# Optimization experiments

Hardware: AMD Instinct MI355X
Metric: run time of the kernel (lower is better)

## Reference

```python
import jax, jax.numpy as jnp
import numpy as np

B, SEQ, PRED, N, PATCH, STRIDE = 4, 720, 720, 64, 16, 8
DM, EL = 256, 2
PNUM = (PRED + SEQ - PATCH) // STRIDE + 2  # 180
EPS = 1e-5


def _gelu(x):
    return jax.nn.gelu(x, approximate=False)  # torch nn.GELU default (erf)


def _ln(x, w, b):
    mu = x.mean(-1, keepdims=True)
    var = ((x - mu) ** 2).mean(-1, keepdims=True)
    return (x - mu) / jnp.sqrt(var + EPS) * w + b


def _pos_emb(n, d):
    pos = np.arange(n)[:, None].astype(np.float32)
    div = np.exp(np.arange(0, d, 2).astype(np.float32) * (-np.log(10000.0) / d))
    pe = np.zeros((n, d), np.float32)
    pe[:, 0::2] = np.sin(pos * div)
    pe[:, 1::2] = np.cos(pos * div)
    return jnp.asarray(pe)


def _patch_embed(x, emb_w):
    # x: [B, N, L]; ReplicationPad1d((0, STRIDE)) then unfold(patch_len, stride)
    xp = jnp.concatenate([x, jnp.repeat(x[..., -1:], STRIDE, axis=-1)], axis=-1)
    npatch = (xp.shape[-1] - PATCH) // STRIDE + 1
    idx = jnp.arange(npatch)[:, None] * STRIDE + jnp.arange(PATCH)[None, :]
    patches = xp[..., idx]  # [B, N, npatch, PATCH]
    emb = jnp.einsum('bnpl,ld->bnpd', patches, emb_w) + _pos_emb(npatch, DM)
    return emb.reshape(-1, npatch, DM)  # [B*N, npatch, DM]


def _temp_mix(x, w1, b1, w2, b2, nw, nb):
    # Pnum independent Linear(DM,DM)->GELU->Linear(DM,DM), residual + LayerNorm
    h = _gelu(jnp.einsum('bpd,pde->bpe', x, w1) + b1[None])
    o = jnp.einsum('bpd,pde->bpe', h, w2) + b2[None]
    return _ln(o + x, nw, nb)


def _chan_mix(x, w1, b1, w2, b2, nw, nb):
    # DM independent Linear(PNUM,PNUM)->GELU->Linear(PNUM,PNUM), residual + LayerNorm
    h = _gelu(jnp.einsum('bpd,dpq->bqd', x, w1) + b1.T[None])
    o = jnp.einsum('bpd,dpq->bqd', h, w2) + b2.T[None]
    return _ln(o + x, nw, nb)


def _s_correction(x, x_pre):
    xf = jnp.fft.rfft(x, axis=1, norm='ortho')
    pf = jnp.fft.rfft(x_pre, axis=1, norm='ortho')
    xi = jnp.maximum(jnp.fft.irfft(xf * jnp.conj(xf), axis=1), 0.0)
    pi = jnp.maximum(jnp.fft.irfft(pf * jnp.conj(pf), axis=1), 0.0)
    alpha = (xi * pi).sum(1, keepdims=True) / ((pi * pi).sum(1, keepdims=True) + 0.001)
    return jnp.sqrt(alpha)


def _forward(history_data, future_data, revin_w, revin_b, pred_w, pred_b, emb_w,
             ln_w, ln_b, comb_w, comb_b, head_w, head_b,
             tmd_w1, tmd_b1, tmd_w2, tmd_b2, tmd_nw, tmd_nb,
             cmd_w1, cmd_b1, cmd_w2, cmd_b2, cmd_nw, cmd_nb,
             tmu_w1, tmu_b1, tmu_w2, tmu_b2, tmu_nw, tmu_nb,
             cmu_w1, cmu_b1, cmu_w2, cmu_b2, cmu_nw, cmu_nb):
    x0 = history_data[:, :, :, 0]  # [B, SEQ, N]
    mean = x0.mean(1, keepdims=True)
    stdev = jnp.sqrt(x0.var(1, keepdims=True) + EPS)  # unbiased=False
    xn = (x0 - mean) / stdev * revin_w + revin_b  # RevIN norm (affine)
    x = jnp.einsum('bln,lt->bnt', xn, pred_w) + pred_b  # predict_linear on [B,N,SEQ]
    xi = _patch_embed(x, emb_w)  # [B*N, PNUM, DM]
    x_old = _patch_embed(jnp.transpose(x0, (0, 2, 1)), emb_w)  # [B*N, P_old, DM]
    x_all = jnp.zeros(xi.shape + (EL,), xi.dtype)
    for li in range(EL):
        xud = _temp_mix(xi, tmd_w1[li], tmd_b1[li], tmd_w2[li], tmd_b2[li], tmd_nw[li], tmd_nb[li])
        xud = _chan_mix(xud, cmd_w1[li], cmd_b1[li], cmd_w2[li], cmd_b2[li], cmd_nw[li], cmd_nb[li])
        for j in range(li, -1, -1):
            xud = _temp_mix(xud, tmu_w1[j], tmu_b1[j], tmu_w2[j], tmu_b2[j], tmu_nw[j], tmu_nb[j])
            xud = _chan_mix(xud, cmu_w1[j], cmu_b1[j], cmu_w2[j], cmu_b2[j], cmu_nw[j], cmu_nb[j])
        # faithful to original: inner loop shadows `i`, so the write index is always 0
        x_all = x_all.at[:, :, :, 0].set(xud)
    xc = jnp.einsum('bpde,e->bpd', x_all, comb_w) + comb_b  # comb: Linear(EL, 1)
    p_old = x_old.shape[1]
    xc = _s_correction(_ln(x_old, ln_w, ln_b), _ln(xc[:, :p_old, :], ln_w, ln_b)) * xc
    xr = xc.reshape(-1, N, PNUM, DM).transpose(0, 1, 3, 2)  # [B, N, DM, PNUM]
    out = xr.reshape(xr.shape[0], N, DM * PNUM) @ head_w + head_b  # Flatten_Head -> [B, N, PRED]
    out = jnp.transpose(out, (0, 2, 1))  # [B, PRED, N]
    out = (out - revin_b) / (revin_w + EPS * EPS) * stdev + mean  # RevIN denorm
    return out[:, -PRED:, :][..., None]  # [B, PRED, N, 1]


def setup_inputs() -> dict:
    key = jax.random.key(0)
    ks = iter(jax.random.split(key, 64))
    f = lambda shape, s=0.02: s * jax.random.normal(next(ks), shape, jnp.float32)
    inp = dict(
        history_data=jax.random.normal(next(ks), (B, SEQ, N, 1), jnp.float32),
        future_data=jax.random.normal(next(ks), (B, PRED, N, 1), jnp.float32),
        batch_seen=0, epoch=0, train=0,
        revin_w=jnp.ones((N,), jnp.float32), revin_b=jnp.zeros((N,), jnp.float32),
        pred_w=f((SEQ, SEQ + PRED)), pred_b=jnp.zeros((SEQ + PRED,), jnp.float32),
        emb_w=f((PATCH, DM)),
        ln_w=jnp.ones((DM,), jnp.float32), ln_b=jnp.zeros((DM,), jnp.float32),
        comb_w=f((EL,), 0.5), comb_b=jnp.zeros((), jnp.float32),
        head_w=f((DM * PNUM, PRED), 0.005), head_b=jnp.zeros((PRED,), jnp.float32),
    )
    for pre in ('tmd', 'tmu'):
        inp[pre + '_w1'] = f((EL, PNUM, DM, DM)); inp[pre + '_b1'] = jnp.zeros((EL, PNUM, DM), jnp.float32)
        inp[pre + '_w2'] = f((EL, PNUM, DM, DM)); inp[pre + '_b2'] = jnp.zeros((EL, PNUM, DM), jnp.float32)
        inp[pre + '_nw'] = jnp.ones((EL, DM), jnp.float32); inp[pre + '_nb'] = jnp.zeros((EL, DM), jnp.float32)
    for pre in ('cmd', 'cmu'):
        inp[pre + '_w1'] = f((EL, DM, PNUM, PNUM)); inp[pre + '_b1'] = jnp.zeros((EL, DM, PNUM), jnp.float32)
        inp[pre + '_w2'] = f((EL, DM, PNUM, PNUM)); inp[pre + '_b2'] = jnp.zeros((EL, DM, PNUM), jnp.float32)
        inp[pre + '_nw'] = jnp.ones((EL, DM), jnp.float32); inp[pre + '_nb'] = jnp.zeros((EL, DM), jnp.float32)
    return inp


def reference(history_data, future_data, revin_w, revin_b, pred_w, pred_b, emb_w,
              ln_w, ln_b, comb_w, comb_b, head_w, head_b,
              tmd_w1, tmd_b1, tmd_w2, tmd_b2, tmd_nw, tmd_nb,
              cmd_w1, cmd_b1, cmd_w2, cmd_b2, cmd_nw, cmd_nb,
              tmu_w1, tmu_b1, tmu_w2, tmu_b2, tmu_nw, tmu_nb,
              cmu_w1, cmu_b1, cmu_w2, cmu_b2, cmu_nw, cmu_nb,
              batch_seen, epoch, train):
    return _forward(history_data, future_data, revin_w, revin_b, pred_w, pred_b, emb_w,
                    ln_w, ln_b, comb_w, comb_b, head_w, head_b,
                    tmd_w1, tmd_b1, tmd_w2, tmd_b2, tmd_nw, tmd_nb,
                    cmd_w1, cmd_b1, cmd_w2, cmd_b2, cmd_nw, cmd_nb,
                    tmu_w1, tmu_b1, tmu_w2, tmu_b2, tmu_nw, tmu_nb,
                    cmu_w1, cmu_b1, cmu_w2, cmu_b2, cmu_nw, cmu_nb)
```

## Files before the change

### kernel.cpp

```cpp
#include <hip/hip_runtime.h>
#include <cstdint>
#include <cstddef>

namespace {

constexpr int SEQ_ = 720;
constexpr int N_ = 64;
constexpr int T_ = 1440;
constexpr int P_ = 180;
constexpr int PO_ = 90;
constexpr int D_ = 256;
constexpr int PD_ = P_ * D_;
constexpr float EPS_ = 1e-5f;
constexpr int NTILE_ = 39744;

typedef __attribute__((ext_vector_type(8))) short bf16x8;
typedef __attribute__((ext_vector_type(4))) float f32x4;
typedef __attribute__((ext_vector_type(4))) unsigned short u16x4;

__device__ __forceinline__ float gelu_exact(float x) {
  return 0.5f * x * (1.0f + erff(x * 0.70710678118654752f));
}

__device__ __forceinline__ unsigned short f2bf(float x) {
// ... 115 lines not shown
      int idx = bn * 90 + p0 + tid;
      muX[idx] = mu;
      rsX[idx] = rsqrtf(Q * (1.f / 256.f) - mu * mu + EPS_);
    }
  }
}

struct TileInfo {
  const float* Wg; unsigned short* Og;
  int K, Nn, Kp, k0, n0;
};

__device__ __forceinline__ TileInfo decode_tile(
    int bid,
    const float* t0, const float* t1, const float* t2, const float* t3,
    const float* t4, const float* t5,
    const float* c0, const float* c1, const float* c2, const float* c3,
    const float* c4p, const float* c5, const float* hw,
    unsigned short* WtAll, unsigned short* WcAll, unsigned short* WhAll) {
  TileInfo ti;
  int tk, tn;
  if (bid < 17280) {
    int tt = bid / 2880, rem = bid - tt * 2880;
    int g = rem >> 4, tile = rem & 15;
    const float* s = t0;
    if (tt == 1) s = t1; else if (tt == 2) s = t2; else if (tt == 3) s = t3;
    else if (tt == 4) s = t4; else if (tt == 5) s = t5;
    ti.Wg = s + (size_t)g * 65536;
    ti.Og = WtAll + (size_t)tt * 11796480 + (size_t)g * 65536;
    ti.K = 256; ti.Nn = 256; ti.Kp = 256; tk = tile >> 2; tn = tile & 3;
  } else if (bid < 31104) {
    int b2 = bid - 17280;
    int tt = b2 / 2304, rem = b2 - tt * 2304;
    int g = rem / 9, tile = rem - g * 9;
    const float* s = c0;
    if (tt == 1) s = c1; else if (tt == 2) s = c2; else if (tt == 3) s = c3;
    else if (tt == 4) s = c4p; else if (tt == 5) s = c5;
    ti.Wg = s + (size_t)g * 32400;
    ti.Og = WcAll + (size_t)tt * 9437184 + (size_t)g * 36864;
    ti.K = 180; ti.Nn = 180; ti.Kp = 192; tk = tile / 3; tn = tile - (tile / 3) * 3;
  } else {
    int b2 = bid - 31104;
    ti.Wg = hw; ti.Og = WhAll;
    ti.K = 46080; ti.Nn = 720; ti.Kp = 46080; tk = b2 / 12; tn = b2 - (b2 / 12) * 12;
  }
  ti.k0 = tk * 64; ti.n0 = tn * 64;
  return ti;
}

__global__ __launch_bounds__(256) void convT_all_kernel(
    const float* t0, const float* t1, const float* t2, const float* t3,
    const float* t4, const float* t5,
    const float* c0, const float* c1, const float* c2, const float* c3,
    const float* c4p, const float* c5,
    const float* hw,
    unsigned short* WtAll, unsigned short* WcAll, unsigned short* WhAll,
    int phase, int step) {
  __shared__ float Ts[2][64][65];
  int tid = threadIdx.x;
  int kr = tid >> 4, nc = (tid & 15) * 4;
  int S = gridDim.x * step;

  auto do_load = [&](const TileInfo& ti, float4* r) {
    #pragma unroll
    for (int i = 0; i < 4; i++) {
      int k = ti.k0 + kr + i * 16;
      float4 v = make_float4(0.f, 0.f, 0.f, 0.f);
      if (k < ti.K) {
        int n = ti.n0 + nc;
        if (n + 3 < ti.Nn) {
          v = *reinterpret_cast<const float4*>(ti.Wg + (size_t)k * ti.Nn + n);
        } else {
          if (n + 0 < ti.Nn) v.x = ti.Wg[(size_t)k * ti.Nn + n + 0];
          if (n + 1 < ti.Nn) v.y = ti.Wg[(size_t)k * ti.Nn + n + 1];
          if (n + 2 < ti.Nn) v.z = ti.Wg[(size_t)k * ti.Nn + n + 2];
          if (n + 3 < ti.Nn) v.w = ti.Wg[(size_t)k * ti.Nn + n + 3];
        }
      }
      r[i] = v;
    }
  };

  auto do_write = [&](const float4* r, int b) {
    #pragma unroll
    for (int i = 0; i < 4; i++) {
      Ts[b][kr + i * 16][nc + 0] = r[i].x;
      Ts[b][kr + i * 16][nc + 1] = r[i].y;
      Ts[b][kr + i * 16][nc + 2] = r[i].z;
      Ts[b][kr + i * 16][nc + 3] = r[i].w;
    }
  };

  auto do_store = [&](const TileInfo& ti, int b) {
    #pragma unroll
    for (int it = 0; it < 2; it++) {
      int nr = (tid >> 3) + it * 32;
      int kc = (tid & 7) * 8;
      unsigned int tmp[4];
      #pragma unroll
      for (int j = 0; j < 4; j++) {
        unsigned int lo = f2bf(Ts[b][kc + 2 * j][nr]);
        unsigned int hi = f2bf(Ts[b][kc + 2 * j + 1][nr]);
        tmp[j] = lo | (hi << 16);
      }
      uint4 vv; vv.x = tmp[0]; vv.y = tmp[1]; vv.z = tmp[2]; vv.w = tmp[3];
      *reinterpret_cast<uint4*>(ti.Og + (size_t)(ti.n0 + nr) * ti.Kp + ti.k0 + kc) = vv;
    }
  };

#define DECODE(tt) decode_tile((tt), t0,t1,t2,t3,t4,t5, c0,c1,c2,c3,c4p,c5, hw, WtAll, WcAll, WhAll)

  int t = phase + blockIdx.x * step;
  if (t >= NTILE_) return;

  float4 rA[4], rB[4];
  TileInfo i0 = DECODE(t);
  do_load(i0, rA);
  bool v1 = (t + S < NTILE_);
  TileInfo i1 = v1 ? DECODE(t + S) : i0;
  if (v1) do_load(i1, rB);
  do_write(rA, 0);
  bool v2 = (t + 2 * S < NTILE_);
  TileInfo i2 = v2 ? DECODE(t + 2 * S) : i0;
  if (v2) do_load(i2, rA);
  __syncthreads();

  while (true) {
    if (v1) do_write(rB, 1);
    {
      bool v3 = (t + 3 * S < NTILE_);
      TileInfo i3 = i2;
      if (v3) { i3 = DECODE(t + 3 * S); do_load(i3, rB); }
      do_store(i0, 0);
      __syncthreads();
      t += S;
      if (!v1) return;
      i0 = i1; i1 = i2; i2 = i3; v1 = v2; v2 = v3;
    }
    if (v1) do_write(rA, 0);
    {
      bool v3 = (t + 3 * S < NTILE_);
      TileInfo i3 = i2;
      if (v3) { i3 = DECODE(t + 3 * S); do_load(i3, rA); }
      do_store(i0, 1);
      __syncthreads();
      t += S;
      if (!v1) return;
      i0 = i1; i1 = i2; i2 = i3; v1 = v2; v2 = v3;
    }
  }
#undef DECODE
}

__global__ __launch_bounds__(256, 3) void temp_mfma_kernel(
    const unsigned short* __restrict__ X, unsigned short* __restrict__ Y,
    const unsigned short* __restrict__ W1t, const float* __restrict__ B1,
    const unsigned short* __restrict__ W2t, const float* __restrict__ B2,
    const float* __restrict__ NW, const float* __restrict__ NB) {
  __shared__ __align__(16) short Xs[64 * 256];
  __shared__ float partS[64][4];
  __shared__ float partQ[64][4];
  int lin = (blockIdx.x & 7) * 90 + (blockIdx.x >> 3);
  int p = lin >> 2;
  int m0 = (lin & 3) << 6;
  int tid = threadIdx.x;
  int w = tid >> 6, l = tid & 63;
  int lr = l & 15, lq = l >> 4;
  int n0w = w << 6;

  const unsigned short* W1p = W1t + (size_t)p * 65536;
  const unsigned short* W2p = W2t + (size_t)p * 65536;

  bf16x8 bhc[4], bhn[4];
  #pragma unroll
  for (int nf = 0; nf < 4; nf++)
    bhc[nf] = *reinterpret_cast<const bf16x8*>(W1p + (size_t)(n0w + nf * 16 + lr) * 256 + lq * 8);

  const unsigned short* Xblk = X + (size_t)m0 * PD_ + (size_t)p * D_;
  for (int i = tid; i < 64 * 32; i += 256) {
    int r = i >> 5, c8 = (i & 31) << 3;
    uint4 v = *reinterpret_cast<const uint4*>(Xblk + (size_t)r * PD_ + c8);
    *reinterpret_cast<uint4*>(&Xs[r * 256 + (c8 ^ ((r & 7) << 3))]) = v;
  }
  __syncthreads();

  f32x4 zero4 = {0.f, 0.f, 0.f, 0.f};
  f32x4 acc[4][4];
  #pragma unroll
  for (int a = 0; a < 4; a++)
    #pragma unroll
    for (int b = 0; b < 4; b++) acc[a][b] = zero4;

  for (int ks = 0; ks < 8; ks++) {
    int kb = ks * 32 + lq * 8;
    bf16x8 af[4];
    #pragma unroll
    for (int mf = 0; mf < 4; mf++) {
      int r = mf * 16 + lr;
      af[mf] = *reinterpret_cast<const bf16x8*>(&Xs[r * 256 + (kb ^ ((r & 7) << 3))]);
    }
    if (ks < 7) {
      #pragma unroll
      for (int nf = 0; nf < 4; nf++)
        bhn[nf] = *reinterpret_cast<const bf16x8*>(W1p + (size_t)(n0w + nf * 16 + lr) * 256 + kb + 32);
    }
    #pragma unroll
    for (int mf = 0; mf < 4; mf++)
      #pragma unroll
      for (int nf = 0; nf < 4; nf++)
        acc[mf][nf] = __builtin_amdgcn_mfma_f32_16x16x32_bf16(af[mf], bhc[nf], acc[mf][nf], 0, 0, 0);
    if (ks < 7) {
      #pragma unroll
      for (int nf = 0; nf < 4; nf++) bhc[nf] = bhn[nf];
    }
  }

  bf16x8 bh2[4];
  #pragma unroll
  for (int nf = 0; nf < 4; nf++)
    bh2[nf] = *reinterpret_cast<const bf16x8*>(W2p + (size_t)(n0w + nf * 16 + lr) * 256 + lq * 8);

  __syncthreads();

  #pragma unroll
  for (int nf = 0; nf < 4; nf++) {
    int n = n0w + nf * 16 + lr;
    float bias = B1[p * 256 + n];
    #pragma unroll
    for (int mf = 0; mf < 4; mf++)
      #pragma unroll
      for (int rg = 0; rg < 4; rg++) {
        int r = mf * 16 + lq * 4 + rg;
        Xs[r * 256 + (n ^ ((r & 7) << 3))] =
            (short)f2bf(gelu_exact(acc[mf][nf][rg] + bias));
      }
  }
  __syncthreads();

  #pragma unroll
  for (int a = 0; a < 4; a++)
    #pragma unroll
    for (int b = 0; b < 4; b++) acc[a][b] = zero4;
  for (int ks = 0; ks < 8; ks++) {
    int kb = ks * 32 + lq * 8;
    bf16x8 af[4];
    #pragma unroll
    for (int mf = 0; mf < 4; mf++) {
      int r = mf * 16 + lr;
      af[mf] = *reinterpret_cast<const bf16x8*>(&Xs[r * 256 + (kb ^ ((r & 7) << 3))]);
    }
    if (ks < 7) {
      #pragma unroll
      for (int nf = 0; nf < 4; nf++)
        bhn[nf] = *reinterpret_cast<const bf16x8*>(W2p + (size_t)(n0w + nf * 16 + lr) * 256 + kb + 32);
    }
    #pragma unroll
    for (int mf = 0; mf < 4; mf++)
      #pragma unroll
      for (int nf = 0; nf < 4; nf++)
        acc[mf][nf] = __builtin_amdgcn_mfma_f32_16x16x32_bf16(af[mf], bh2[nf], acc[mf][nf], 0, 0, 0);
    if (ks < 7) {
      #pragma unroll
      for (int nf = 0; nf < 4; nf++) bh2[nf] = bhn[nf];
    }
  }

  __syncthreads();

  for (int i = tid; i < 64 * 32; i += 256) {
    int r = i >> 5, c8 = (i & 31) << 3;
    uint4 v = *reinterpret_cast<const uint4*>(Xblk + (size_t)r * PD_ + c8);
    *reinterpret_cast<uint4*>(&Xs[r * 256 + (c8 ^ ((r & 7) << 3))]) = v;
  }
  __syncthreads();

  float b2v[4], nwv[4], nbv[4];
  #pragma unroll
  for (int nf = 0; nf < 4; nf++) {
    int n = n0w + nf * 16 + lr;
    b2v[nf] = B2[p * 256 + n];
    nwv[nf] = NW[n];
    nbv[nf] = NB[n];
  }
  #pragma unroll
  for (int nf = 0; nf < 4; nf++) {
    int n = n0w + nf * 16 + lr;
    #pragma unroll
    for (int mf = 0; mf < 4; mf++)
      #pragma unroll
      for (int rg = 0; rg < 4; rg++) {
        int r = mf * 16 + lq * 4 + rg;
        float res = bf2f((unsigned short)Xs[r * 256 + (n ^ ((r & 7) << 3))]);
        acc[mf][nf][rg] += b2v[nf] + res;
      }
  }
  #pragma unroll
  for (int mf = 0; mf < 4; mf++)
    #pragma unroll
    for (int rg = 0; rg < 4; rg++) {
      float s = acc[mf][0][rg] + acc[mf][1][rg] + acc[mf][2][rg] + acc[mf][3][rg];
      float q = acc[mf][0][rg] * acc[mf][0][rg] + acc[mf][1][rg] * acc[mf][1][rg] +
                acc[mf][2][rg] * acc[mf][2][rg] + acc[mf][3][rg] * acc[mf][3][rg];
      #pragma unroll
      for (int off = 1; off < 16; off <<= 1) {
        s += __shfl_xor(s, off);
        q += __shfl_xor(q, off);
      }
      if (lr == 0) {
        int r = mf * 16 + lq * 4 + rg;
        partS[r][w] = s;
        partQ[r][w] = q;
      }
    }
  __syncthreads();
  #pragma unroll
  for (int mf = 0; mf < 4; mf++)
    #pragma unroll
    for (int rg = 0; rg < 4; rg++) {
      int r = mf * 16 + lq * 4 + rg;
      float S = partS[r][0] + partS[r][1] + partS[r][2] + partS[r][3];
      float Q = partQ[r][0] + partQ[r][1] + partQ[r][2] + partQ[r][3];
      float mu = S * (1.f / 256.f);
      float rstd = rsqrtf(Q * (1.f / 256.f) - mu * mu + EPS_);
      #pragma unroll
      for (int nf = 0; nf < 4; nf++) {
        int n = n0w + nf * 16 + lr;
        Xs[r * 256 + (n ^ ((r & 7) << 3))] =
            (short)f2bf((acc[mf][nf][rg] - mu) * rstd * nwv[nf] + nbv[nf]);
      }
    }
  __syncthreads();
  unsigned short* Yblk = Y + (size_t)m0 * PD_ + (size_t)p * D_;
  for (int i = tid; i < 64 * 32; i += 256) {
    int r = i >> 5, c8 = (i & 31) << 3;
    uint4 v = *reinterpret_cast<uint4*>(&Xs[r * 256 + (c8 ^ ((r & 7) << 3))]);
    *reinterpret_cast<uint4*>(Yblk + (size_t)r * PD_ + c8) = v;
  }
}

__global__ __launch_bounds__(256) void tr_AB_kernel(
    const unsigned short* __restrict__ A, unsigned short* __restrict__ B16) {
  __shared__ unsigned short T[32][184];
  int bn = blockIdx.y;
  int d0 = blockIdx.x * 32;
  int tid = threadIdx.x;
  int ld = tid & 31, pw = tid >> 5;
  for (int p = pw; p < 180; p += 8)
    T[ld][p] = A[((size_t)bn * 180 + p) * 256 + d0 + ld];
  __syncthreads();
  unsigned int* Bu = reinterpret_cast<unsigned int*>(B16);
  for (int i = tid; i < 32 * 96; i += 256) {
    int r = i / 96, jj = i - r * 96;
    int p0 = 2 * jj;
    unsigned int lo = (p0 < 180) ? (unsigned int)T[r][p0] : 0u;
    unsigned int hi = (p0 + 1 < 180) ? (unsigned int)T[r][p0 + 1] : 0u;
    Bu[((size_t)bn * 256 + d0 + r) * 96 + jj] = lo | (hi << 16);
  }
}

__global__ __launch_bounds__(256, 3) void chan_mfma_kernel(
    const unsigned short* __restrict__ Xb, unsigned short* __restrict__ Yb,
    const unsigned short* __restrict__ W1t, const float* __restrict__ B1,
    const unsigned short* __restrict__ W2t, const float* __restrict__ B2) {
  __shared__ __align__(16) short Xs[64 * 200];
  int lin = (blockIdx.x & 7) * 128 + (blockIdx.x >> 3);
  int d = lin >> 2;
  int m0 = (lin & 3) << 6;
  int tid = threadIdx.x;
  int w = tid >> 6, l = tid & 63;
  int lr = l & 15, lq = l >> 4;
  int n0w = w * 48;

  const unsigned short* W1p = W1t + (size_t)d * (192 * 192);
  const unsigned short* W2p = W2t + (size_t)d * (192 * 192);

  bf16x8 bhc[3], bhn[3];
  #pragma unroll
  for (int nf = 0; nf < 3; nf++)
    bhc[nf] = *reinterpret_cast<const bf16x8*>(W1p + (size_t)(n0w + nf * 16 + lr) * 192 + lq * 8);

  for (int i = tid; i < 64 * 24; i += 256) {
    int r = i / 24, c = i - r * 24;
    uint4 v = *reinterpret_cast<const uint4*>(
        Xb + ((size_t)(m0 + r) * 256 + d) * 192 + c * 8);
    *reinterpret_cast<uint4*>(&Xs[r * 200 + c * 8]) = v;
  }
  __syncthreads();

  f32x4 zero4 = {0.f, 0.f, 0.f, 0.f};
  f32x4 acc[4][3];
  #pragma unroll
  for (int a = 0; a < 4; a++)
    #pragma unroll
    for (int b = 0; b < 3; b++) acc[a][b] = zero4;

  for (int ks = 0; ks < 6; ks++) {
    int kb = ks * 32 + lq * 8;
    bf16x8 af[4];
    #pragma unroll
    for (int mf = 0; mf < 4; mf++)
      af[mf] = *reinterpret_cast<const bf16x8*>(&Xs[(mf * 16 + lr) * 200 + kb]);
    if (ks < 5) {
      #pragma unroll
      for (int nf = 0; nf < 3; nf++)
        bhn[nf] = *reinterpret_cast<const bf16x8*>(W1p + (size_t)(n0w + nf * 16 + lr) * 192 + kb + 32);
    }
    #pragma unroll
    for (int mf = 0; mf < 4; mf++)
      #pragma unroll
      for (int nf = 0; nf < 3; nf++)
        acc[mf][nf] = __builtin_amdgcn_mfma_f32_16x16x32_bf16(af[mf], bhc[nf], acc[mf][nf], 0, 0, 0);
    if (ks < 5) {
      #pragma unroll
      for (int nf = 0; nf < 3; nf++) bhc[nf] = bhn[nf];
    }
  }

  bf16x8 bh2[3];
  #pragma unroll
  for (int nf = 0; nf < 3; nf++)
    bh2[nf] = *reinterpret_cast<const bf16x8*>(W2p + (size_t)(n0w + nf * 16 + lr) * 192 + lq * 8);

  __syncthreads();

  #pragma unroll
  for (int nf = 0; nf < 3; nf++) {
    int n = n0w + nf * 16 + lr;
    bool valid = n < 180;
    float bias = valid ? B1[d * 180 + n] : 0.f;
    #pragma unroll
    for (int mf = 0; mf < 4; mf++)
      #pragma unroll
      for (int rg = 0; rg < 4; rg++) {
        int r = mf * 16 + lq * 4 + rg;
        float h = valid ? gelu_exact(acc[mf][nf][rg] + bias) : 0.f;
        Xs[r * 200 + n] = (short)f2bf(h);
      }
  }
  __syncthreads();

  #pragma unroll
  for (int a = 0; a < 4; a++)
    #pragma unroll
    for (int b = 0; b < 3; b++) acc[a][b] = zero4;
  for (int ks = 0; ks < 6; ks++) {
    int kb = ks * 32 + lq * 8;
    bf16x8 af[4];
    #pragma unroll
    for (int mf = 0; mf < 4; mf++)
      af[mf] = *reinterpret_cast<const bf16x8*>(&Xs[(mf * 16 + lr) * 200 + kb]);
    if (ks < 5) {
      #pragma unroll
      for (int nf = 0; nf < 3; nf++)
        bhn[nf] = *reinterpret_cast<const bf16x8*>(W2p + (size_t)(n0w + nf * 16 + lr) * 192 + kb + 32);
    }
    #pragma unroll
    for (int mf = 0; mf < 4; mf++)
      #pragma unroll
      for (int nf = 0; nf < 3; nf++)
        acc[mf][nf] = __builtin_amdgcn_mfma_f32_16x16x32_bf16(af[mf], bh2[nf], acc[mf][nf], 0, 0, 0);
    if (ks < 5) {
      #pragma unroll
      for (int nf = 0; nf < 3; nf++) bh2[nf] = bhn[nf];
    }
  }

  __syncthreads();

  for (int i = tid; i < 64 * 24; i += 256) {
    int r = i / 24, c = i - r * 24;
    uint4 v = *reinterpret_cast<const uint4*>(
        Xb + ((size_t)(m0 + r) * 256 + d) * 192 + c * 8);
    *reinterpret_cast<uint4*>(&Xs[r * 200 + c * 8]) = v;
  }
  __syncthreads();

  #pragma unroll
  for (int nf = 0; nf < 3; nf++) {
    int n = n0w + nf * 16 + lr;
    if (n < 180) {
      float b2v = B2[d * 180 + n];
      #pragma unroll
      for (int mf = 0; mf < 4; mf++)
        #pragma unroll
        for (int rg = 0; rg < 4; rg++) {
          int r = mf * 16 + lq * 4 + rg;
          float res = bf2f((unsigned short)Xs[r * 200 + n]);
          Yb[((size_t)(m0 + r) * 256 + d) * 180 + n] = f2bf(acc[mf][nf][rg] + b2v + res);
        }
    }
  }
}

__global__ __launch_bounds__(256) void trLN_kernel(
    const unsigned short* __restrict__ Bsrc, unsigned short* __restrict__ A,
    const float* __restrict__ nw, const float* __restrict__ nb,
    const float* __restrict__ cw, const float* __restrict__ cb, int useComb,
    float* __restrict__ muP, float* __restrict__ rsP) {
  __shared__ float Tl[16][260];
  int bn = blockIdx.y;
  int p0 = blockIdx.x * 16;
  int tid = threadIdx.x;
  int j = tid & 15, db = tid >> 4;
  #pragma unroll 4
  for (int it = 0; it < 16; ++it) {
    int dd = it * 16 + db;
    float v = 0.f;
    if (p0 + j < 180)
      v = bf2f(Bsrc[((size_t)(bn * 256) + dd) * 180 + p0 + j]);
    Tl[j][dd] = v;
  }
  __syncthreads();
  int w = tid >> 6, l = tid & 63;
  float scale = 1.f, shift = 0.f;
  if (useComb) { scale = cw[0]; shift = cb[0]; }
  float4 w4 = *reinterpret_cast<const float4*>(nw + l * 4);
  float4 b4 = *reinterpret_cast<const float4*>(nb + l * 4);
  #pragma unroll
  for (int rr = 0; rr < 4; ++rr) {
    int row = w * 4 + rr;
    int p = p0 + row;
    float4 v = *reinterpret_cast<const float4*>(&Tl[row][l * 4]);
    float s = v.x + v.y + v.z + v.w;
    float s2 = v.x*v.x + v.y*v.y + v.z*v.z + v.w*v.w;
    #pragma unroll
    for (int off = 32; off > 0; off >>= 1) { s += __shfl_xor(s, off); s2 += __shfl_xor(s2, off); }
    float mu = s * (1.f/256.f);
    float rstd = rsqrtf(s2 * (1.f/256.f) - mu * mu + EPS_);
    if (p < 180) {
      float o0 = ((v.x - mu) * rstd * w4.x + b4.x) * scale + shift;
      float o1 = ((v.y - mu) * rstd * w4.y + b4.y) * scale + shift;
      float o2 = ((v.z - mu) * rstd * w4.z + b4.z) * scale + shift;
      float o3 = ((v.w - mu) * rstd * w4.w + b4.w) * scale + shift;
      unsigned int w0 = (unsigned int)f2bf(o0) | ((unsigned int)f2bf(o1) << 16);
      unsigned int w1 = (unsigned int)f2bf(o2) | ((unsigned int)f2bf(o3) << 16);
      unsigned int* dst = reinterpret_cast<unsigned int*>(
          A + ((size_t)bn * 180 + p) * 256 + l * 4);
      dst[0] = w0; dst[1] = w1;
      if (useComb && p < 90) {
        float so = o0 + o1 + o2 + o3;
        float qo = o0*o0 + o1*o1 + o2*o2 + o3*o3;
        #pragma unroll
        for (int off = 32; off > 0; off >>= 1) { so += __shfl_xor(so, off); qo += __shfl_xor(qo, off); }
        if (l == 0) {
          float muo = so * (1.f/256.f);
          muP[bn * 90 + p] = muo;
          rsP[bn * 90 + p] = rsqrtf(qo * (1.f/256.f) - muo * muo + EPS_);
        }
      }
    }
  }
}

__global__ __launch_bounds__(128, 1) void autocorr_kernel(
    const unsigned short* __restrict__ xoldB, const unsigned short* __restrict__ xcB,
    const float* __restrict__ muX, const float* __restrict__ rsX,
    const float* __restrict__ muP, const float* __restrict__ rsP,
    const float* __restrict__ lnw, const float* __restrict__ lnb,
    float* __restrict__ sqa) {
  __shared__ float PI[46][64];
  __shared__ float RED[2][2][64];
  int bn = blockIdx.x >> 2;
  int tid = threadIdx.x;
  int dl = tid & 63;
  int half = tid >> 6;
  int j0 = half * 23;
  int d = ((blockIdx.x & 3) << 6) + dl;
  float w = lnw[d], bb = lnb[d];
  float v[90], wr[90];

  {
    const unsigned short* col = xcB + (size_t)bn * PD_ + d;
    const float* m = muP + bn * 90;
    const float* rs = rsP + bn * 90;
    #pragma unroll
    for (int p = 0; p < 90; p++)
      v[p] = (bf2f(col[(size_t)p * D_]) - m[p]) * rs[p] * w + bb;
    #pragma unroll
    for (int p = 0; p < 90; p++)
      wr[p] = (half == 0) ? v[p] : v[(p + 23) % 90];
  }
  float den = 0.f;
  #pragma unroll 1
  for (int jt = 0; jt < 24; jt += 4) {
    float c0 = 0.f, c1 = 0.f, c2 = 0.f, c3 = 0.f;
    #pragma unroll
    for (int mm = 0; mm < 90; mm++) {
      float vm = v[mm];
      c0 += vm * wr[mm];
      c1 += vm * ((mm + 1 < 90) ? wr[mm + 1] : wr[mm - 89]);
      c2 += vm * ((mm + 2 < 90) ? wr[mm + 2] : wr[mm - 88]);
      c3 += vm * ((mm + 3 < 90) ? wr[mm + 3] : wr[mm - 87]);
    }
    float cq[4] = {c0, c1, c2, c3};
    #pragma unroll
    for (int q = 0; q < 4; q++) {
      if (jt + q < 23) {
        int lag = j0 + jt + q;
        float piv = fmaxf(cq[q] * 0.10540925533894598f, 0.f);
        PI[lag][dl] = piv;
        float wgt = (lag == 0 || lag == 45) ? 1.f : 2.f;
        den += wgt * piv * piv;
      }
    }
    float t0 = wr[0], t1 = wr[1], t2 = wr[2], t3 = wr[3];
    #pragma unroll
    for (int mm = 0; mm < 86; mm++) wr[mm] = wr[mm + 4];
    wr[86] = t0; wr[87] = t1; wr[88] = t2; wr[89] = t3;
  }

  {
    const unsigned short* col = xoldB + (size_t)bn * (PO_ * D_) + d;
    const float* m = muX + bn * 90;
    const float* rs = rsX + bn * 90;
    #pragma unroll
    for (int p = 0; p < 90; p++)
      v[p] = (bf2f(col[(size_t)p * D_]) - m[p]) * rs[p] * w + bb;
    #pragma unroll
    for (int p = 0; p < 90; p++)
      wr[p] = (half == 0) ? v[p] : v[(p + 23) % 90];
  }
  float num = 0.f;
  #pragma unroll 1
  for (int jt = 0; jt < 24; jt += 4) {
    float c0 = 0.f, c1 = 0.f, c2 = 0.f, c3 = 0.f;
    #pragma unroll
    for (int mm = 0; mm < 90; mm++) {
      float vm = v[mm];
      c0 += vm * wr[mm];
      c1 += vm * ((mm + 1 < 90) ? wr[mm + 1] : wr[mm - 89]);
      c2 += vm * ((mm + 2 < 90) ? wr[mm + 2] : wr[mm - 88]);
      c3 += vm * ((mm + 3 < 90) ? wr[mm + 3] : wr[mm - 87]);
    }
    float cq[4] = {c0, c1, c2, c3};
    #pragma unroll
    for (int q = 0; q < 4; q++) {
// ... 80 lines not shown
      bhc[nf] = *reinterpret_cast<const bf16x8*>(Bw + (size_t)(n0 + nf * 16 + lr) * 46080 + kb);
  }
  for (int s = w; s < 90; s += 4) {
    int sn = s + 4;
    if (sn < 90) {
      size_t kb = kbase + (size_t)sn * 32 + lq * 8;
      #pragma unroll
      for (int mf = 0; mf < 4; mf++)
        afn[mf] = *reinterpret_cast<const bf16x8*>(A + (size_t)(m0 + mf * 16 + lr) * 46080 + kb);
      #pragma unroll
      for (int nf = 0; nf < 4; nf++)
        bhn[nf] = *reinterpret_cast<const bf16x8*>(Bw + (size_t)(n0 + nf * 16 + lr) * 46080 + kb);
    }
    #pragma unroll
    for (int mf = 0; mf < 4; mf++)
      #pragma unroll
      for (int nf = 0; nf < 4; nf++)
        acc[mf][nf] = __builtin_amdgcn_mfma_f32_16x16x32_bf16(afc[mf], bhc[nf], acc[mf][nf], 0, 0, 0);
    if (sn < 90) {
      #pragma unroll
      for (int mf = 0; mf < 4; mf++) afc[mf] = afn[mf];
      #pragma unroll
      for (int nf = 0; nf < 4; nf++) bhc[nf] = bhn[nf];
    }
  }
  for (int ww = 0; ww < 4; ww++) {
    if (w == ww) {
      #pragma unroll
      for (int mf = 0; mf < 4; mf++)
        #pragma unroll
        for (int nf = 0; nf < 4; nf++)
          #pragma unroll
          for (int rg = 0; rg < 4; rg++) {
            int r = mf * 16 + lq * 4 + rg, c = nf * 16 + lr;
            if (ww == 0) Rs[r][c] = acc[mf][nf][rg];
            else Rs[r][c] += acc[mf][nf][rg];
          }
    }
    __syncthreads();
  }
  for (int i = tid; i < 64 * 64; i += 256) {
    int r = i >> 6, c = i & 63;
    int n = n0 + c;
    if (n < 720)
      P[((size_t)ks * 256 + m0 + r) * 720 + n] = Rs[r][c];
  }
}

__global__ __launch_bounds__(256) void final_kernel(
    const float* __restrict__ P, const float* __restrict__ hb,
    const float* __restrict__ rw, const float* __restrict__ rb,
    const float* __restrict__ meanA, const float* __restrict__ stdevA,
    float* __restrict__ out) {
  int gid = blockIdx.x * 256 + threadIdx.x;
  int bn = gid / 720, t = gid - bn * 720;
  float s = 0.f;
  #pragma unroll
  for (int ks = 0; ks < 16; ks++) s += P[(size_t)ks * 184320 + gid];
  s += hb[t];
  int b = bn >> 6, n = bn & 63;
  float val = (s - rb[n]) / (rw[n] + 1e-10f) * stdevA[bn] + meanA[bn];
  out[((size_t)(b * 720 + t)) * 64 + n] = val;
}

}

extern "C" void kernel_launch(void* const* d_in, const int* in_sizes, int n_in,
                              void* d_out, int out_size, void* d_ws, size_t ws_size,
                              hipStream_t stream) {
  (void)in_sizes; (void)n_in; (void)out_size; (void)ws_size;
  const float* hist   = (const float*)d_in[0];
  const float* revw   = (const float*)d_in[5];
  const float* revb   = (const float*)d_in[6];
  const float* predw  = (const float*)d_in[7];
  const float* predb  = (const float*)d_in[8];
  const float* embw   = (const float*)d_in[9];
  const float* lnw    = (const float*)d_in[10];
  const float* lnb    = (const float*)d_in[11];
  const float* combw  = (const float*)d_in[12];
  const float* combb  = (const float*)d_in[13];
  const float* headw  = (const float*)d_in[14];
  const float* headb  = (const float*)d_in[15];
  const float* tmd_w1 = (const float*)d_in[16];
  const float* tmd_b1 = (const float*)d_in[17];
  const float* tmd_w2 = (const float*)d_in[18];
  const float* tmd_b2 = (const float*)d_in[19];
  const float* tmd_nw = (const float*)d_in[20];
  const float* tmd_nb = (const float*)d_in[21];
  const float* tmu_w1 = (const float*)d_in[22];
  const float* tmu_b1 = (const float*)d_in[23];
  const float* tmu_w2 = (const float*)d_in[24];
  const float* tmu_b2 = (const float*)d_in[25];
  const float* tmu_nw = (const float*)d_in[26];
  const float* tmu_nb = (const float*)d_in[27];
  const float* cmd_w1 = (const float*)d_in[28];
  const float* cmd_b1 = (const float*)d_in[29];
  const float* cmd_w2 = (const float*)d_in[30];
  const float* cmd_b2 = (const float*)d_in[31];
  const float* cmd_nw = (const float*)d_in[32];
  const float* cmd_nb = (const float*)d_in[33];
  const float* cmu_w1 = (const float*)d_in[34];
  const float* cmu_b1 = (const float*)d_in[35];
  const float* cmu_w2 = (const float*)d_in[36];
  const float* cmu_b2 = (const float*)d_in[37];
  const float* cmu_nw = (const float*)d_in[38];
  const float* cmu_nb = (const float*)d_in[39];

  float* ws = (float*)d_ws;
  float* meanA  = ws;
  float* stdevA = meanA + 256;
  float* sA     = stdevA + 256;
  float* sB     = sA + 256;
  float* muX    = sB + 256;
  float* rsX    = muX + 23040;
  float* muP    = rsX + 23040;
  float* rsP    = muP + 23040;
  float* sqa    = rsP + 23040;
  float* xbuf   = sqa + 65536;
  unsigned short* xoldB = (unsigned short*)(xbuf + 368640);
  unsigned short* A0    = xoldB + 5898240;
  unsigned short* A1    = A0 + 11796480;
  unsigned short* B16   = A1 + 11796480;
  unsigned short* Yb    = B16 + 12582912;
  float* part           = (float*)(Yb + 11796480);
  unsigned short* Xtb   = (unsigned short*)(part + 2949120);
  unsigned short* WtAll = Xtb + 11796480;
  unsigned short* WcAll = WtAll + 70778880;
  unsigned short* WhAll = WcAll + 56623104;

  constexpr int TW = 180 * 256 * 256, TB = 180 * 256;
  constexpr int CW = 256 * 180 * 180, CB = 256 * 180;
  constexpr size_t TSTR = 11796480, CSTR = 9437184;

  convT_all_kernel<<<2048, 256, 0, stream>>>(
      tmd_w1 + TW, tmd_w2 + TW, tmu_w1 + TW, tmu_w2 + TW, tmu_w1, tmu_w2,
      cmd_w1 + CW, cmd_w2 + CW, cmu_w1 + CW, cmu_w2 + CW, cmu_w1, cmu_w2,
      headw, WtAll, WcAll, WhAll, 0, 1);

  revin_stats_kernel<<<4, 256, 0, stream>>>(hist, revw, revb, meanA, stdevA, sA, sB);
  pred_kernel<<<dim3(45, 4), 256, 0, stream>>>(hist, predw, predb, sA, sB, xbuf);
  embed_kernel<<<dim3(12, 256), 256, 0, stream>>>(xbuf, embw, A0, 0, nullptr, nullptr);
  embed_kernel<<<dim3(6, 256), 256, 0, stream>>>(hist, embw, xoldB, 1, muX, rsX);

  const float* tB1[3] = {tmd_b1 + TB, tmu_b1 + TB, tmu_b1};
  const float* tB2[3] = {tmd_b2 + TB, tmu_b2 + TB, tmu_b2};
  const float* tNW[3] = {tmd_nw + 256, tmu_nw + 256, tmu_nw};
  const float* tNB[3] = {tmd_nb + 256, tmu_nb + 256, tmu_nb};
  const float* cB1[3] = {cmd_b1 + CB, cmu_b1 + CB, cmu_b1};
  const float* cB2[3] = {cmd_b2 + CB, cmu_b2 + CB, cmu_b2};
  const float* cNW[3] = {cmd_nw + 256, cmu_nw + 256, cmu_nw};
  const float* cNB[3] = {cmd_nb + 256, cmu_nb + 256, cmu_nb};

  for (int li = 0; li < 3; li++) {
    temp_mfma_kernel<<<720, 256, 0, stream>>>(
        A0, A1, WtAll + (size_t)(2 * li) * TSTR, tB1[li],
        WtAll + (size_t)(2 * li + 1) * TSTR, tB2[li], tNW[li], tNB[li]);
    tr_AB_kernel<<<dim3(8, 256), 256, 0, stream>>>(A1, B16);
    chan_mfma_kernel<<<1024, 256, 0, stream>>>(
        B16, Yb, WcAll + (size_t)(2 * li) * CSTR, cB1[li],
        WcAll + (size_t)(2 * li + 1) * CSTR, cB2[li]);
    trLN_kernel<<<dim3(12, 256), 256, 0, stream>>>(Yb, A0, cNW[li], cNB[li],
                                                   combw, combb, li == 2 ? 1 : 0,
                                                   muP, rsP);
  }

  autocorr_kernel<<<1024, 128, 0, stream>>>(xoldB, A0, muX, rsX, muP, rsP, lnw, lnb, sqa);
  scale_tr_kernel<<<dim3(48, 256), 256, 0, stream>>>(A0, sqa, Xtb);
  head_mfma_kernel<<<768, 256, 0, stream>>>(Xtb, WhAll, part);
  final_kernel<<<720, 256, 0, stream>>>(part, headb, revw, revb, meanA, stdevA, (float*)d_out);
}
```

Measured before the change: 1.111 ms.

## Halve M-tile in temp/chan MFMA kernels to double blocks and occupancy

The temporal and channel mixing MFMA kernels now process 32 rows per block instead of 64, doubling the grid size and halving shared memory and accumulator registers so more blocks fit per CU. The weight register double-buffering prefetch is removed in favour of loading weight fragments at the top of each k-step. The cost is that each weight fragment is now read from global/L2 by twice as many blocks, and there is less MFMA work per load to hide latency.

```diff
diff --git a/kernel.cpp b/kernel.cpp
--- a/kernel.cpp
+++ b/kernel.cpp
@@ -291,17 +291,17 @@
 #undef DECODE
 }
 
-__global__ __launch_bounds__(256, 3) void temp_mfma_kernel(
+__global__ __launch_bounds__(256, 6) void temp_mfma_kernel(
     const unsigned short* __restrict__ X, unsigned short* __restrict__ Y,
     const unsigned short* __restrict__ W1t, const float* __restrict__ B1,
     const unsigned short* __restrict__ W2t, const float* __restrict__ B2,
     const float* __restrict__ NW, const float* __restrict__ NB) {
-  __shared__ __align__(16) short Xs[64 * 256];
-  __shared__ float partS[64][4];
-  __shared__ float partQ[64][4];
-  int lin = (blockIdx.x & 7) * 90 + (blockIdx.x >> 3);
-  int p = lin >> 2;
-  int m0 = (lin & 3) << 6;
+  __shared__ __align__(16) short Xs[32 * 256];
+  __shared__ float partS[32][4];
+  __shared__ float partQ[32][4];
+  int lin = (blockIdx.x & 7) * 180 + (blockIdx.x >> 3);
+  int p = lin >> 3;
+  int m0 = (lin & 7) << 5;
   int tid = threadIdx.x;
   int w = tid >> 6, l = tid & 63;
   int lr = l & 15, lq = l >> 4;
@@ -310,13 +310,8 @@
   const unsigned short* W1p = W1t + (size_t)p * 65536;
   const unsigned short* W2p = W2t + (size_t)p * 65536;
 
-  bf16x8 bhc[4], bhn[4];
-  #pragma unroll
-  for (int nf = 0; nf < 4; nf++)
-    bhc[nf] = *reinterpret_cast<const bf16x8*>(W1p + (size_t)(n0w + nf * 16 + lr) * 256 + lq * 8);
-
   const unsigned short* Xblk = X + (size_t)m0 * PD_ + (size_t)p * D_;
-  for (int i = tid; i < 64 * 32; i += 256) {
+  for (int i = tid; i < 32 * 32; i += 256) {
     int r = i >> 5, c8 = (i & 31) << 3;
     uint4 v = *reinterpret_cast<const uint4*>(Xblk + (size_t)r * PD_ + c8);
     *reinterpret_cast<uint4*>(&Xs[r * 256 + (c8 ^ ((r & 7) << 3))]) = v;
@@ -324,41 +319,30 @@
   __syncthreads();
 
   f32x4 zero4 = {0.f, 0.f, 0.f, 0.f};
-  f32x4 acc[4][4];
-  #pragma unroll
-  for (int a = 0; a < 4; a++)
+  f32x4 acc[2][4];
+  #pragma unroll
+  for (int a = 0; a < 2; a++)
     #pragma unroll
     for (int b = 0; b < 4; b++) acc[a][b] = zero4;
 
   for (int ks = 0; ks < 8; ks++) {
     int kb = ks * 32 + lq * 8;
-    bf16x8 af[4];
-    #pragma unroll
-    for (int mf = 0; mf < 4; mf++) {
+    bf16x8 bh[4];
+    #pragma unroll
+    for (int nf = 0; nf < 4; nf++)
+      bh[nf] = *reinterpret_cast<const bf16x8*>(W1p + (size_t)(n0w + nf * 16 + lr) * 256 + kb);
+    bf16x8 af[2];
+    #pragma unroll
+    for (int mf = 0; mf < 2; mf++) {
       int r = mf * 16 + lr;
       af[mf] = *reinterpret_cast<const bf16x8*>(&Xs[r * 256 + (kb ^ ((r & 7) << 3))]);
     }
-    if (ks < 7) {
+    #pragma unroll
+    for (int mf = 0; mf < 2; mf++)
       #pragma unroll
       for (int nf = 0; nf < 4; nf++)
-        bhn[nf] = *reinterpret_cast<const bf16x8*>(W1p + (size_t)(n0w + nf * 16 + lr) * 256 + kb + 32);
-    }
-    #pragma unroll
-    for (int mf = 0; mf < 4; mf++)
-      #pragma unroll
-      for (int nf = 0; nf < 4; nf++)
-        acc[mf][nf] = __builtin_amdgcn_mfma_f32_16x16x32_bf16(af[mf], bhc[nf], acc[mf][nf], 0, 0, 0);
-    if (ks < 7) {
-      #pragma unroll
-      for (int nf = 0; nf < 4; nf++) bhc[nf] = bhn[nf];
-    }
-  }
-
-  bf16x8 bh2[4];
-  #pragma unroll
-  for (int nf = 0; nf < 4; nf++)
-    bh2[nf] = *reinterpret_cast<const bf16x8*>(W2p + (size_t)(n0w + nf * 16 + lr) * 256 + lq * 8);
-
+        acc[mf][nf] = __builtin_amdgcn_mfma_f32_16x16x32_bf16(af[mf], bh[nf], acc[mf][nf], 0, 0, 0);
+  }
   __syncthreads();
 
   #pragma unroll
@@ -366,7 +350,7 @@
     int n = n0w + nf * 16 + lr;
     float bias = B1[p * 256 + n];
     #pragma unroll
-    for (int mf = 0; mf < 4; mf++)
+    for (int mf = 0; mf < 2; mf++)
       #pragma unroll
       for (int rg = 0; rg < 4; rg++) {
         int r = mf * 16 + lq * 4 + rg;
@@ -377,36 +361,30 @@
   __syncthreads();
 
   #pragma unroll
-  for (int a = 0; a < 4; a++)
+  for (int a = 0; a < 2; a++)
     #pragma unroll
     for (int b = 0; b < 4; b++) acc[a][b] = zero4;
   for (int ks = 0; ks < 8; ks++) {
     int kb = ks * 32 + lq * 8;
-    bf16x8 af[4];
-    #pragma unroll
-    for (int mf = 0; mf < 4; mf++) {
+    bf16x8 bh[4];
+    #pragma unroll
+    for (int nf = 0; nf < 4; nf++)
+      bh[nf] = *reinterpret_cast<const bf16x8*>(W2p + (size_t)(n0w + nf * 16 + lr) * 256 + kb);
+    bf16x8 af[2];
+    #pragma unroll
+    for (int mf = 0; mf < 2; mf++) {
       int r = mf * 16 + lr;
       af[mf] = *reinterpret_cast<const bf16x8*>(&Xs[r * 256 + (kb ^ ((r & 7) << 3))]);
     }
-    if (ks < 7) {
+    #pragma unroll
+    for (int mf = 0; mf < 2; mf++)
       #pragma unroll
       for (int nf = 0; nf < 4; nf++)
-        bhn[nf] = *reinterpret_cast<const bf16x8*>(W2p + (size_t)(n0w + nf * 16 + lr) * 256 + kb + 32);
-    }
-    #pragma unroll
-    for (int mf = 0; mf < 4; mf++)
-      #pragma unroll
-      for (int nf = 0; nf < 4; nf++)
-        acc[mf][nf] = __builtin_amdgcn_mfma_f32_16x16x32_bf16(af[mf], bh2[nf], acc[mf][nf], 0, 0, 0);
-    if (ks < 7) {
-      #pragma unroll
-      for (int nf = 0; nf < 4; nf++) bh2[nf] = bhn[nf];
-    }
-  }
-
-  __syncthreads();
-
-  for (int i = tid; i < 64 * 32; i += 256) {
+        acc[mf][nf] = __builtin_amdgcn_mfma_f32_16x16x32_bf16(af[mf], bh[nf], acc[mf][nf], 0, 0, 0);
+  }
+  __syncthreads();
+
+  for (int i = tid; i < 32 * 32; i += 256) {
     int r = i >> 5, c8 = (i & 31) << 3;
     uint4 v = *reinterpret_cast<const uint4*>(Xblk + (size_t)r * PD_ + c8);
     *reinterpret_cast<uint4*>(&Xs[r * 256 + (c8 ^ ((r & 7) << 3))]) = v;
@@ -425,7 +403,7 @@
   for (int nf = 0; nf < 4; nf++) {
     int n = n0w + nf * 16 + lr;
     #pragma unroll
-    for (int mf = 0; mf < 4; mf++)
+    for (int mf = 0; mf < 2; mf++)
       #pragma unroll
       for (int rg = 0; rg < 4; rg++) {
         int r = mf * 16 + lq * 4 + rg;
@@ -434,7 +412,7 @@
       }
   }
   #pragma unroll
-  for (int mf = 0; mf < 4; mf++)
+  for (int mf = 0; mf < 2; mf++)
     #pragma unroll
     for (int rg = 0; rg < 4; rg++) {
       float s = acc[mf][0][rg] + acc[mf][1][rg] + acc[mf][2][rg] + acc[mf][3][rg];
@@ -453,7 +431,7 @@
     }
   __syncthreads();
   #pragma unroll
-  for (int mf = 0; mf < 4; mf++)
+  for (int mf = 0; mf < 2; mf++)
     #pragma unroll
     for (int rg = 0; rg < 4; rg++) {
       int r = mf * 16 + lq * 4 + rg;
@@ -470,7 +448,7 @@
     }
   __syncthreads();
   unsigned short* Yblk = Y + (size_t)m0 * PD_ + (size_t)p * D_;
-  for (int i = tid; i < 64 * 32; i += 256) {
+  for (int i = tid; i < 32 * 32; i += 256) {
     int r = i >> 5, c8 = (i & 31) << 3;
     uint4 v = *reinterpret_cast<uint4*>(&Xs[r * 256 + (c8 ^ ((r & 7) << 3))]);
     *reinterpret_cast<uint4*>(Yblk + (size_t)r * PD_ + c8) = v;
@@ -497,14 +475,14 @@
   }
 }
 
-__global__ __launch_bounds__(256, 3) void chan_mfma_kernel(
+__global__ __launch_bounds__(256, 6) void chan_mfma_kernel(
     const unsigned short* __restrict__ Xb, unsigned short* __restrict__ Yb,
     const unsigned short* __restrict__ W1t, const float* __restrict__ B1,
     const unsigned short* __restrict__ W2t, const float* __restrict__ B2) {
-  __shared__ __align__(16) short Xs[64 * 200];
-  int lin = (blockIdx.x & 7) * 128 + (blockIdx.x >> 3);
-  int d = lin >> 2;
-  int m0 = (lin & 3) << 6;
+  __shared__ __align__(16) short Xs[32 * 200];
+  int lin = (blockIdx.x & 7) * 256 + (blockIdx.x >> 3);
+  int d = lin >> 3;
+  int m0 = (lin & 7) << 5;
   int tid = threadIdx.x;
   int w = tid >> 6, l = tid & 63;
   int lr = l & 15, lq = l >> 4;
@@ -513,12 +491,7 @@
   const unsigned short* W1p = W1t + (size_t)d * (192 * 192);
   const unsigned short* W2p = W2t + (size_t)d * (192 * 192);
 
-  bf16x8 bhc[3], bhn[3];
-  #pragma unroll
-  for (int nf = 0; nf < 3; nf++)
-    bhc[nf] = *reinterpret_cast<const bf16x8*>(W1p + (size_t)(n0w + nf * 16 + lr) * 192 + lq * 8);
-
-  for (int i = tid; i < 64 * 24; i += 256) {
+  for (int i = tid; i < 32 * 24; i += 256) {
     int r = i / 24, c = i - r * 24;
     uint4 v = *reinterpret_cast<const uint4*>(
         Xb + ((size_t)(m0 + r) * 256 + d) * 192 + c * 8);
@@ -527,39 +500,28 @@
   __syncthreads();
 
   f32x4 zero4 = {0.f, 0.f, 0.f, 0.f};
-  f32x4 acc[4][3];
-  #pragma unroll
-  for (int a = 0; a < 4; a++)
+  f32x4 acc[2][3];
+  #pragma unroll
+  for (int a = 0; a < 2; a++)
     #pragma unroll
     for (int b = 0; b < 3; b++) acc[a][b] = zero4;
 
   for (int ks = 0; ks < 6; ks++) {
     int kb = ks * 32 + lq * 8;
-    bf16x8 af[4];
-    #pragma unroll
-    for (int mf = 0; mf < 4; mf++)
+    bf16x8 bh[3];
+    #pragma unroll
+    for (int nf = 0; nf < 3; nf++)
+      bh[nf] = *reinterpret_cast<const bf16x8*>(W1p + (size_t)(n0w + nf * 16 + lr) * 192 + kb);
+    bf16x8 af[2];
+    #pragma unroll
+    for (int mf = 0; mf < 2; mf++)
       af[mf] = *reinterpret_cast<const bf16x8*>(&Xs[(mf * 16 + lr) * 200 + kb]);
-    if (ks < 5) {
+    #pragma unroll
+    for (int mf = 0; mf < 2; mf++)
       #pragma unroll
       for (int nf = 0; nf < 3; nf++)
-        bhn[nf] = *reinterpret_cast<const bf16x8*>(W1p + (size_t)(n0w + nf * 16 + lr) * 192 + kb + 32);
-    }
-    #pragma unroll
-    for (int mf = 0; mf < 4; mf++)
-      #pragma unroll
-      for (int nf = 0; nf < 3; nf++)
-        acc[mf][nf] = __builtin_amdgcn_mfma_f32_16x16x32_bf16(af[mf], bhc[nf], acc[mf][nf], 0, 0, 0);
-    if (ks < 5) {
-      #pragma unroll
-      for (int nf = 0; nf < 3; nf++) bhc[nf] = bhn[nf];
-    }
-  }
-
-  bf16x8 bh2[3];
-  #pragma unroll
-  for (int nf = 0; nf < 3; nf++)
-    bh2[nf] = *reinterpret_cast<const bf16x8*>(W2p + (size_t)(n0w + nf * 16 + lr) * 192 + lq * 8);
-
+        acc[mf][nf] = __builtin_amdgcn_mfma_f32_16x16x32_bf16(af[mf], bh[nf], acc[mf][nf], 0, 0, 0);
+  }
   __syncthreads();
 
   #pragma unroll
@@ -568,7 +530,7 @@
     bool valid = n < 180;
     float bias = valid ? B1[d * 180 + n] : 0.f;
     #pragma unroll
-    for (int mf = 0; mf < 4; mf++)
+    for (int mf = 0; mf < 2; mf++)
       #pragma unroll
       for (int rg = 0; rg < 4; rg++) {
         int r = mf * 16 + lq * 4 + rg;
@@ -579,34 +541,28 @@
   __syncthreads();
 
   #pragma unroll
-  for (int a = 0; a < 4; a++)
+  for (int a = 0; a < 2; a++)
     #pragma unroll
     for (int b = 0; b < 3; b++) acc[a][b] = zero4;
   for (int ks = 0; ks < 6; ks++) {
     int kb = ks * 32 + lq * 8;
-    bf16x8 af[4];
-    #pragma unroll
-    for (int mf = 0; mf < 4; mf++)
+    bf16x8 bh[3];
+    #pragma unroll
+    for (int nf = 0; nf < 3; nf++)
+      bh[nf] = *reinterpret_cast<const bf16x8*>(W2p + (size_t)(n0w + nf * 16 + lr) * 192 + kb);
+    bf16x8 af[2];
+    #pragma unroll
+    for (int mf = 0; mf < 2; mf++)
       af[mf] = *reinterpret_cast<const bf16x8*>(&Xs[(mf * 16 + lr) * 200 + kb]);
-    if (ks < 5) {
+    #pragma unroll
+    for (int mf = 0; mf < 2; mf++)
       #pragma unroll
       for (int nf = 0; nf < 3; nf++)
-        bhn[nf] = *reinterpret_cast<const bf16x8*>(W2p + (size_t)(n0w + nf * 16 + lr) * 192 + kb + 32);
-    }
-    #pragma unroll
-    for (int mf = 0; mf < 4; mf++)
-      #pragma unroll
-      for (int nf = 0; nf < 3; nf++)
-        acc[mf][nf] = __builtin_amdgcn_mfma_f32_16x16x32_bf16(af[mf], bh2[nf], acc[mf][nf], 0, 0, 0);
-    if (ks < 5) {
-      #pragma unroll
-      for (int nf = 0; nf < 3; nf++) bh2[nf] = bhn[nf];
-    }
-  }
-
-  __syncthreads();
-
-  for (int i = tid; i < 64 * 24; i += 256) {
+        acc[mf][nf] = __builtin_amdgcn_mfma_f32_16x16x32_bf16(af[mf], bh[nf], acc[mf][nf], 0, 0, 0);
+  }
+  __syncthreads();
+
+  for (int i = tid; i < 32 * 24; i += 256) {
     int r = i / 24, c = i - r * 24;
     uint4 v = *reinterpret_cast<const uint4*>(
         Xb + ((size_t)(m0 + r) * 256 + d) * 192 + c * 8);
@@ -620,7 +576,7 @@
     if (n < 180) {
       float b2v = B2[d * 180 + n];
       #pragma unroll
-      for (int mf = 0; mf < 4; mf++)
+      for (int mf = 0; mf < 2; mf++)
         #pragma unroll
         for (int rg = 0; rg < 4; rg++) {
           int r = mf * 16 + lq * 4 + rg;
@@ -1007,11 +963,11 @@
   const float* cNB[3] = {cmd_nb + 256, cmu_nb + 256, cmu_nb};
 
   for (int li = 0; li < 3; li++) {
-    temp_mfma_kernel<<<720, 256, 0, stream>>>(
+    temp_mfma_kernel<<<1440, 256, 0, stream>>>(
         A0, A1, WtAll + (size_t)(2 * li) * TSTR, tB1[li],
         WtAll + (size_t)(2 * li + 1) * TSTR, tB2[li], tNW[li], tNB[li]);
     tr_AB_kernel<<<dim3(8, 256), 256, 0, stream>>>(A1, B16);
-    chan_mfma_kernel<<<1024, 256, 0, stream>>>(
+    chan_mfma_kernel<<<2048, 256, 0, stream>>>(
         B16, Yb, WcAll + (size_t)(2 * li) * CSTR, cB1[li],
         WcAll + (size_t)(2 * li + 1) * CSTR, cB2[li]);
     trLN_kernel<<<dim3(12, 256), 256, 0, stream>>>(Yb, A0, cNW[li], cNB[li],
```

After: 1.170 ms. 1.05x slower.
